# Kernel tuning notes

Hardware: AMD Instinct MI355X
Metric: run time of the kernel (lower is better)

Reference implementation:

```python
import jax, jax.numpy as jnp
import numpy as np

B, Q, E = 4, 1024, 1024
N_HEAD, D_HEAD = 16, 64
LN_EPS = 1e-3  # keras LayerNormalization default


def rel_shift(x):
    # x: [b, q, k, n] -> Transformer-XL relative shift along k axis
    b, q, k, n = x.shape
    x = jnp.pad(x, ((0, 0), (0, 0), (1, 0), (0, 0)))
    x = x.reshape(b, k + 1, q, n)[:, 1:]
    return x.reshape(b, q, k, n)


def setup_inputs() -> dict:
    key = jax.random.key(0)
    ks = jax.random.split(key, 12)
    s = 0.02
    w = jax.random.normal(ks[0], (B, Q, E), jnp.float32)
    r = jax.random.normal(ks[1], (Q, E), jnp.float32)
    r_w_bias = jax.random.normal(ks[2], (N_HEAD, D_HEAD), jnp.float32) * s
    r_r_bias = jax.random.normal(ks[3], (N_HEAD, D_HEAD), jnp.float32) * s
    # causal mask: 1 where j > i (masked), float as in original
    idx = jnp.arange(Q)
    attn_mask = (idx[None, :] > idx[:, None]).astype(jnp.float32)
    Wq = jax.random.normal(ks[4], (E, N_HEAD * D_HEAD), jnp.float32) * s
    Wk = jax.random.normal(ks[5], (E, N_HEAD * D_HEAD), jnp.float32) * s
    Wv = jax.random.normal(ks[6], (E, N_HEAD * D_HEAD), jnp.float32) * s
    Wr = jax.random.normal(ks[7], (E, N_HEAD * D_HEAD), jnp.float32) * s
    Wo = jax.random.normal(ks[8], (N_HEAD * D_HEAD, E), jnp.float32) * s
    gamma = jnp.ones((E,), jnp.float32)
    beta = jnp.zeros((E,), jnp.float32)
    return {"w": w, "r": r, "r_w_bias": r_w_bias, "r_r_bias": r_r_bias,
            "attn_mask": attn_mask, "Wq": Wq, "Wk": Wk, "Wv": Wv, "Wr": Wr,
            "Wo": Wo, "gamma": gamma, "beta": beta}


def reference(w, r, r_w_bias, r_r_bias, attn_mask, Wq, Wk, Wv, Wr, Wo, gamma, beta):
    b, q_len, embed = w.shape
    r_len = r.shape[0]
    # QKV / R projections (use_bias=False)
    q = (w @ Wq).reshape(b, q_len, N_HEAD, D_HEAD)
    k = (w @ Wk).reshape(b, q_len, N_HEAD, D_HEAD)
    v = (w @ Wv).reshape(b, q_len, N_HEAD, D_HEAD)
    rp = (r @ Wr).reshape(r_len, N_HEAD, D_HEAD)
    rw_q = q + r_w_bias  # [b,i,n,d]
    rr_q = q + r_r_bias
    AC = jnp.einsum('bind,bjnd->bijn', rw_q, k)
    BD = jnp.einsum('bind,jnd->bijn', rr_q, rp)
    BD = rel_shift(BD)
    attention = (AC + BD) / jnp.sqrt(jnp.float32(embed))
    m = attn_mask[None, :, :, None]
    attention = attention * (1.0 - m) - 1e30 * m
    attn_score = jax.nn.softmax(attention, axis=-2)  # softmax over j (key axis)
    out = jnp.einsum('bijn,bjnd->bind', attn_score, v)
    out = out.reshape(b, q_len, N_HEAD * D_HEAD) @ Wo
    x = w + out
    # keras LayerNormalization over last axis
    mu = jnp.mean(x, axis=-1, keepdims=True)
    var = jnp.var(x, axis=-1, keepdims=True)
    x = (x - mu) * jax.lax.rsqrt(var + LN_EPS) * gamma + beta
    return x
```

## Files before the change

### kernel.cpp

```cpp
#include <hip/hip_runtime.h>
#include <math.h>

#define BQ 4
#define SEQ 1024
#define EMB 1024
#define NH 16
#define DH 64
#define LN_EPS 1e-3f

typedef unsigned short u16;
typedef __attribute__((ext_vector_type(8))) unsigned short ushort8;
typedef __attribute__((ext_vector_type(4))) unsigned short ushort4v;
typedef __attribute__((ext_vector_type(8))) __bf16 bf16x8;
typedef __attribute__((ext_vector_type(4))) float f32x4;

__device__ __forceinline__ u16 f2bf(float f) {
  union { float f; unsigned u; } v;
  v.f = f;
  unsigned u = v.u;
  u += 0x7FFF + ((u >> 16) & 1);
  return (u16)(u >> 16);
}
__device__ __forceinline__ float bf2f(u16 h) {
  union { unsigned u; float f; } v;
  v.u = ((unsigned)h) << 16;
  return v.f;
}
__device__ __forceinline__ bf16x8 as_bf(ushort8 v) {
  union { ushort8 u; bf16x8 b; } x;
  x.u = v;
  return x.b;
}
__device__ __forceinline__ f32x4 mfma16(ushort8 a, ushort8 b, f32x4 c) {
  return __builtin_amdgcn_mfma_f32_16x16x32_bf16(as_bf(a), as_bf(b), c, 0, 0, 0);
}
__device__ __forceinline__ void gload16(const u16* g, u16* l) {
  __builtin_amdgcn_global_load_lds(
      (const __attribute__((address_space(1))) void*)g,
      (__attribute__((address_space(3))) void*)l, 16, 0, 0);
}

__global__ __launch_bounds__(256) void prep_kernel(
    const float* __restrict__ w, const float* __restrict__ r,
    const float* __restrict__ Wq, const float* __restrict__ Wk,
    const float* __restrict__ Wv, const float* __restrict__ Wr,
    const float* __restrict__ Wo, u16* __restrict__ wbf,
    u16* __restrict__ rbf, u16* __restrict__ WqkvT, u16* __restrict__ WrT,
    u16* __restrict__ WoT) {
  __shared__ u16 tile[32][33];
  const int bid = blockIdx.x;
  const int tid = threadIdx.x;
  if (bid < 5120) {
    const float* src = (bid < 4096) ? w : r;
    u16* dst = (bid < 4096) ? wbf : rbf;
    const int base = (bid < 4096) ? bid : bid - 4096;
    const int idx = (base * 256 + tid) * 4;
    const float4 v = *(const float4*)&src[idx];
    ushort4v o;
    o[0] = f2bf(v.x);
    o[1] = f2bf(v.y);
    o[2] = f2bf(v.z);
    o[3] = f2bf(v.w);
    *(ushort4v*)&dst[idx] = o;
  } else {
    const int t = bid - 5120;
    const int z = t >> 10;
    const int tt = t & 1023;
    const float* src = (z == 0) ? Wq : (z == 1) ? Wk : (z == 2) ? Wv
                       : (z == 3) ? Wr : Wo;
    u16* dst = (z < 3) ? (WqkvT + (size_t)z * 1024 * 1024)
               : (z == 3) ? WrT : WoT;
    const int k0 = (tt >> 5) * 32, n0 = (tt & 31) * 32;
    const int rr = tid >> 3, c4 = tid & 7;
    const float4 v =
        *(const float4*)&src[(size_t)(k0 + rr) * 1024 + n0 + c4 * 4];
    tile[rr][c4 * 4 + 0] = f2bf(v.x);
    tile[rr][c4 * 4 + 1] = f2bf(v.y);
    tile[rr][c4 * 4 + 2] = f2bf(v.z);
    tile[rr][c4 * 4 + 3] = f2bf(v.w);
    __syncthreads();
    ushort4v o;
#pragma unroll
    for (int e = 0; e < 4; ++e) o[e] = tile[c4 * 4 + e][rr];
    *(ushort4v*)&dst[(size_t)(n0 + rr) * 1024 + k0 + c4 * 4] = o;
  }
}

__device__ __forceinline__ void gemm_core(const u16* __restrict__ A,
                                          const u16* __restrict__ Bt, int bm0,
                                          int bn0, u16* As, u16* Bs, int tid,
                                          f32x4 acc[4][4]) {
  const int quad = (tid >> 4) & 3, colL = tid & 15;
  const int wv = tid >> 6;
  const int wr = wv >> 1, wc = wv & 1;
  const int xs = colL & 7;
  for (int k0 = 0; k0 < 1024; k0 += 64) {
#pragma unroll
    for (int rr = 0; rr < 4; ++rr) {
      const int c = rr * 256 + tid;
      const int row = c >> 3, kc = c & 7;
      const int g = kc ^ (row & 7);
      gload16(&A[(size_t)(bm0 + row) * 1024 + k0 + g * 8], &As[c * 8]);
      gload16(&Bt[(size_t)(bn0 + row) * 1024 + k0 + g * 8], &Bs[c * 8]);
    }
    __syncthreads();
#pragma unroll
    for (int kh = 0; kh < 2; ++kh) {
      const int xo = ((kh * 4 + quad) ^ xs) * 8;
      ushort8 af[4], bf[4];
#pragma unroll
      for (int t = 0; t < 4; ++t) {
        af[t] = *(const ushort8*)&As[(wr * 64 + t * 16 + colL) * 64 + xo];
        bf[t] = *(const ushort8*)&Bs[(wc * 64 + t * 16 + colL) * 64 + xo];
      }
#pragma unroll
      for (int i = 0; i < 4; ++i)
#pragma unroll
        for (int j = 0; j < 4; ++j)
          acc[i][j] = mfma16(af[i], bf[j], acc[i][j]);
    }
    __syncthreads();
  }
}

__global__ __launch_bounds__(256) void gemm_qkvrp(
    const u16* __restrict__ wbf, const u16* __restrict__ WqkvT,
    const u16* __restrict__ rbf, const u16* __restrict__ WrT,
    u16* __restrict__ qk, u16* __restrict__ vT, u16* __restrict__ rpb) {
  __shared__ u16 As[128 * 64];
  __shared__ u16 Bs[128 * 64];
  const int bid = blockIdx.x;
  const int tid = threadIdx.x;
  const bool isR = (bid >= 768);
  const u16* A = isR ? rbf : wbf;
  const u16* Bt = isR ? WrT : WqkvT;
  const int bm0 = isR ? ((bid - 768) >> 3) * 128 : (bid / 24) * 128;
  const int bn0 = isR ? ((bid - 768) & 7) * 128 : (bid % 24) * 128;

  f32x4 acc[4][4] = {};
  gemm_core(A, Bt, bm0, bn0, As, Bs, tid, acc);

  const int quad = (tid >> 4) & 3, colL = tid & 15;
  const int wv = tid >> 6;
  const int wr = wv >> 1, wc = wv & 1;
  const bool vpart = !isR && (bn0 >= 2048);
#pragma unroll
  for (int i = 0; i < 4; ++i) {
    const int grow0 = bm0 + wr * 64 + i * 16 + quad * 4;
#pragma unroll
    for (int j = 0; j < 4; ++j) {
      const int gcol = bn0 + wc * 64 + j * 16 + colL;
      if (vpart) {
        const size_t base =
            ((size_t)(grow0 >> 10) * 1024 + (gcol - 2048)) * 1024 +
            (grow0 & 1023);
        ushort4v o;
#pragma unroll
        for (int e = 0; e < 4; ++e) o[e] = f2bf(acc[i][j][e]);
        *(ushort4v*)&vT[base] = o;
      } else {
        u16* dst = isR ? rpb : qk;
        const int Nld = isR ? 1024 : 2048;
#pragma unroll
        for (int e = 0; e < 4; ++e)
          dst[(size_t)(grow0 + e) * Nld + gcol] = f2bf(acc[i][j][e]);
      }
    }
  }
}

__global__ __launch_bounds__(256) void gemm_wo(const u16* __restrict__ A,
                                               const u16* __restrict__ Bt,
                                               const float* __restrict__ res,
                                               float* __restrict__ C) {
  __shared__ u16 As[128 * 64];
  __shared__ u16 Bs[128 * 64];
  const int tid = threadIdx.x;
  const int bm0 = blockIdx.y * 128, bn0 = blockIdx.x * 128;
  f32x4 acc[4][4] = {};
  gemm_core(A, Bt, bm0, bn0, As, Bs, tid, acc);
  const int quad = (tid >> 4) & 3, colL = tid & 15;
  const int wv = tid >> 6;
  const int wr = wv >> 1, wc = wv & 1;
#pragma unroll
  for (int i = 0; i < 4; ++i) {
    const int grow0 = bm0 + wr * 64 + i * 16 + quad * 4;
#pragma unroll
    for (int j = 0; j < 4; ++j) {
      const int gcol = bn0 + wc * 64 + j * 16 + colL;
#pragma unroll
      for (int e = 0; e < 4; ++e) {
        const size_t off = (size_t)(grow0 + e) * 1024 + gcol;
        C[off] = acc[i][j][e] + res[off];
      }
    }
  }
}

__global__ __launch_bounds__(256, 3) void attn_mfma(
    const u16* __restrict__ qk,
    const u16* __restrict__ vT,
    const u16* __restrict__ rp,
    const float* __restrict__ rwb, const float* __restrict__ rrb,
    u16* __restrict__ obuf) {
  __shared__ u16 smem[22016];
  u16* ks = smem;
  u16* vs = smem + 4096;
  u16* rs = smem + 8192;
  u16* Ps = smem + 16384;

  const int L = blockIdx.x;
  const int b = L & 3;
  const int hn = (L >> 2) & 15;
  const int ph = L >> 6;
  const int itile = (ph < 8) ? ph : 23 - ph;
  const int i0 = itile * 64;
  const int tid = threadIdx.x;
  const int wv = tid >> 6;
  const int lane = tid & 63;
  const int quad = (tid >> 4) & 3, colL = tid & 15;
  u16* Psw = Ps + wv * 16 * 88;
  const int xo0 = (quad ^ (colL & 7)) * 8;
  const int xo1 = ((4 + quad) ^ (colL & 7)) * 8;

  ushort8 qw[2], qr[2];
  {
    const size_t qrow = (size_t)(b * SEQ + i0 + wv * 16 + colL) * 2048;
#pragma unroll
    for (int kh = 0; kh < 2; ++kh) {
      const int dof = hn * 64 + kh * 32 + quad * 8;
      const ushort8 qv = *(const ushort8*)&qk[qrow + dof];
      const float4 w0 = *(const float4*)&rwb[dof];
      const float4 w1 = *(const float4*)&rwb[dof + 4];
      const float4 r0 = *(const float4*)&rrb[dof];
      const float4 r1 = *(const float4*)&rrb[dof + 4];
      const float wb[8] = {w0.x, w0.y, w0.z, w0.w, w1.x, w1.y, w1.z, w1.w};
      const float rb[8] = {r0.x, r0.y, r0.z, r0.w, r1.x, r1.y, r1.z, r1.w};
#pragma unroll
      for (int e = 0; e < 8; ++e) {
        const float qf = bf2f(qv[e]);
        qw[kh][e] = f2bf(qf + wb[e]);
        qr[kh][e] = f2bf(qf + rb[e]);
      }
    }
  }

  {
    const int pb0 = SEQ - 64 - i0;
#pragma unroll
    for (int rr = 0; rr < 2; ++rr) {
      const int c = rr * 256 + tid;
      const int row = c >> 3, gp = c & 7;
      const int g = gp ^ (row & 7);
      gload16(&rp[(size_t)(pb0 + row) * 1024 + hn * 64 + g * 8], &rs[c * 8]);
    }
  }

  f32x4 oacc[4] = {};
  float l_part[4] = {0.f, 0.f, 0.f, 0.f};

  for (int j0 = 0; j0 <= i0; j0 += 64) {
    const int parity = (j0 >> 6) & 1;
    __syncthreads();
#pragma unroll
    for (int rr = 0; rr < 2; ++rr) {
      const int c = rr * 256 + tid;
      const int row = c >> 3, gp = c & 7;
      const int g = gp ^ (row & 7);
      gload16(&qk[(size_t)(b * SEQ + j0 + row) * 2048 + 1024 + hn * 64 + g * 8],
              &ks[c * 8]);
    }
#pragma unroll
    for (int rr = 0; rr < 2; ++rr) {
      const int c = rr * 256 + tid;
      const int d = c >> 3, gp = c & 7;
      const int g = gp ^ (d & 7);
      gload16(&vT[(size_t)(b * SEQ + hn * 64 + d) * 1024 + j0 + g * 8],
              &vs[c * 8]);
    }
    {
      const int pb64 = SEQ - i0 + j0;
      u16* rsH = rs + (parity ^ 1) * 4096;
#pragma unroll
      for (int rr = 0; rr < 2; ++rr) {
        const int c = rr * 256 + tid;
        const int row = c >> 3, gp = c & 7;
        const int g = gp ^ (row & 7);
        int p = pb64 + row;
        p = (p < SEQ) ? p : SEQ - 1;
        gload16(&rp[(size_t)p * 1024 + hn * 64 + g * 8], &rsH[c * 8]);
      }
    }
    __syncthreads();

    f32x4 sAC[4] = {};
#pragma unroll
    for (int jt = 0; jt < 4; ++jt) {
      const int rbase = (jt * 16 + colL) * 64;
      sAC[jt] = mfma16(qw[0], *(const ushort8*)&ks[rbase + xo0], sAC[jt]);
      sAC[jt] = mfma16(qw[1], *(const ushort8*)&ks[rbase + xo1], sAC[jt]);
    }
    f32x4 bd[5];
#pragma unroll
    for (int u = 0; u < 5; ++u) {
      const int tt = 3 - wv + u;
      const int half = ((tt >> 2) ^ parity) & 1;
      const int rbase = half * 4096 + ((tt & 3) * 16 + colL) * 64;
      f32x4 t = {};
      t = mfma16(qr[0], *(const ushort8*)&rs[rbase + xo0], t);
      t = mfma16(qr[1], *(const ushort8*)&rs[rbase + xo1], t);
      bd[u] = t;
    }

#pragma unroll
    for (int r = 0; r < 4; ++r) {
      const int lr = quad * 4 + r;
      const int ig = i0 + wv * 16 + lr;
      const int src = (lane & 48) | ((colL + 15 - lr) & 15);
      float Rv[5];
#pragma unroll
      for (int u = 0; u < 5; ++u) Rv[u] = __shfl(bd[u][r], src, 64);
#pragma unroll
      for (int jt = 0; jt < 4; ++jt) {
        const float bdv = (colL > lr) ? Rv[jt + 1] : Rv[jt];
        const float s = (sAC[jt][r] + bdv) * 0.03125f;
        const float pv = (j0 + jt * 16 + colL <= ig) ? __expf(s - 6.0f) : 0.0f;
        l_part[r] += pv;
        Psw[lr * 88 + jt * 16 + colL] = f2bf(pv);
      }
    }

    const int prow = colL * 88;
#pragma unroll
    for (int dt = 0; dt < 4; ++dt) {
      const int vbase = (dt * 16 + colL) * 64;
      oacc[dt] = mfma16(*(const ushort8*)&Psw[prow + quad * 8],
                        *(const ushort8*)&vs[vbase + xo0], oacc[dt]);
      oacc[dt] = mfma16(*(const ushort8*)&Psw[prow + 32 + quad * 8],
                        *(const ushort8*)&vs[vbase + xo1], oacc[dt]);
    }
  }

#pragma unroll
  for (int r = 0; r < 4; ++r) {
    float l = l_part[r];
    l += __shfl_xor(l, 1);
    l += __shfl_xor(l, 2);
    l += __shfl_xor(l, 4);
    l += __shfl_xor(l, 8);
    const float invl = 1.0f / l;
    const size_t grow =
        (size_t)(b * SEQ + i0 + wv * 16 + quad * 4 + r) * 1024 + hn * 64;
#pragma unroll
    for (int dt = 0; dt < 4; ++dt)
      obuf[grow + dt * 16 + colL] = f2bf(oacc[dt][r] * invl);
  }
}

__global__ __launch_bounds__(256) void ln_kernel(const float* __restrict__ x,
                                                 const float* __restrict__ gamma,
                                                 const float* __restrict__ beta,
                                                 float* __restrict__ out) {
  const int row = blockIdx.x;
  const int tid = threadIdx.x;
  const float4 xv = *(const float4*)&x[(size_t)row * EMB + tid * 4];
  float sum = xv.x + xv.y + xv.z + xv.w;
  float ss = xv.x * xv.x + xv.y * xv.y + xv.z * xv.z + xv.w * xv.w;
#pragma unroll
  for (int off = 1; off < 64; off <<= 1) {
    sum += __shfl_xor(sum, off);
    ss += __shfl_xor(ss, off);
  }
  __shared__ float s1[4], s2[4];
  if ((tid & 63) == 0) {
    s1[tid >> 6] = sum;
    s2[tid >> 6] = ss;
  }
  __syncthreads();
  sum = s1[0] + s1[1] + s1[2] + s1[3];
  ss = s2[0] + s2[1] + s2[2] + s2[3];
  const float mu = sum * (1.f / EMB);
  const float var = ss * (1.f / EMB) - mu * mu;
  const float rstd = rsqrtf(var + LN_EPS);
  const float4 g = *(const float4*)&gamma[tid * 4];
  const float4 be = *(const float4*)&beta[tid * 4];
  float4 o;
  o.x = (xv.x - mu) * rstd * g.x + be.x;
  o.y = (xv.y - mu) * rstd * g.y + be.y;
  o.z = (xv.z - mu) * rstd * g.z + be.z;
  o.w = (xv.w - mu) * rstd * g.w + be.w;
  *(float4*)&out[(size_t)row * EMB + tid * 4] = o;
}

extern "C" void kernel_launch(void* const* d_in, const int* in_sizes, int n_in,
                              void* d_out, int out_size, void* d_ws,
                              size_t ws_size, hipStream_t stream) {
  const float* w = (const float*)d_in[0];
  const float* r = (const float*)d_in[1];
  const float* rwb = (const float*)d_in[2];
  const float* rrb = (const float*)d_in[3];
  const float* Wq = (const float*)d_in[5];
  const float* Wk = (const float*)d_in[6];
  const float* Wv = (const float*)d_in[7];
  const float* Wr = (const float*)d_in[8];
  const float* Wo = (const float*)d_in[9];
  const float* gamma = (const float*)d_in[10];
  const float* beta = (const float*)d_in[11];
  float* outp = (float*)d_out;

  char* wsb = (char*)d_ws;
  u16* wbf = (u16*)(wsb);
  u16* rbf = (u16*)(wsb + ((size_t)8 << 20));
  u16* WqkvT = (u16*)(wsb + ((size_t)10 << 20));
  u16* WrT = (u16*)(wsb + ((size_t)16 << 20));
  u16* WoT = (u16*)(wsb + ((size_t)18 << 20));
  u16* qk = (u16*)(wsb + ((size_t)20 << 20));
  u16* vT = (u16*)(wsb + ((size_t)36 << 20));
  u16* rpb = (u16*)(wsb + ((size_t)44 << 20));
  u16* obuf = (u16*)(wsb + ((size_t)10 << 20));

  const dim3 blk(256);
  prep_kernel<<<10240, blk, 0, stream>>>(w, r, Wq, Wk, Wv, Wr, Wo, wbf, rbf,
                                         WqkvT, WrT, WoT);
  gemm_qkvrp<<<832, blk, 0, stream>>>(wbf, WqkvT, rbf, WrT, qk, vT, rpb);
  attn_mfma<<<1024, blk, 0, stream>>>(qk, vT, rpb, rwb, rrb, obuf);
  gemm_wo<<<dim3(8, 32), blk, 0, stream>>>(obuf, WoT, w, outp);
  ln_kernel<<<BQ * SEQ, blk, 0, stream>>>(outp, gamma, beta, outp);
}
```

Measured before the change: 225.2 us.

## Double-buffer GEMM shared-memory tiles to overlap global loads with MFMA

```diff
diff --git a/kernel.cpp b/kernel.cpp
--- a/kernel.cpp
+++ b/kernel.cpp
@@ -86,40 +86,57 @@
   }
 }
 
-__device__ __forceinline__ void gemm_core(const u16* __restrict__ A,
-                                          const u16* __restrict__ Bt, int bm0,
-                                          int bn0, u16* As, u16* Bs, int tid,
-                                          f32x4 acc[4][4]) {
+__device__ __forceinline__ void gemm_stage(const u16* __restrict__ A,
+                                           const u16* __restrict__ Bt, int bm0,
+                                           int bn0, int k0, u16* As, u16* Bs,
+                                           int tid) {
+#pragma unroll
+  for (int rr = 0; rr < 4; ++rr) {
+    const int c = rr * 256 + tid;
+    const int row = c >> 3, kc = c & 7;
+    const int g = kc ^ (row & 7);
+    gload16(&A[(size_t)(bm0 + row) * 1024 + k0 + g * 8], &As[c * 8]);
+    gload16(&Bt[(size_t)(bn0 + row) * 1024 + k0 + g * 8], &Bs[c * 8]);
+  }
+}
+
+__device__ __forceinline__ void gemm_compute(const u16* As, const u16* Bs,
+                                             int tid, f32x4 acc[4][4]) {
   const int quad = (tid >> 4) & 3, colL = tid & 15;
   const int wv = tid >> 6;
   const int wr = wv >> 1, wc = wv & 1;
   const int xs = colL & 7;
-  for (int k0 = 0; k0 < 1024; k0 += 64) {
-#pragma unroll
-    for (int rr = 0; rr < 4; ++rr) {
-      const int c = rr * 256 + tid;
-      const int row = c >> 3, kc = c & 7;
-      const int g = kc ^ (row & 7);
-      gload16(&A[(size_t)(bm0 + row) * 1024 + k0 + g * 8], &As[c * 8]);
-      gload16(&Bt[(size_t)(bn0 + row) * 1024 + k0 + g * 8], &Bs[c * 8]);
-    }
+#pragma unroll
+  for (int kh = 0; kh < 2; ++kh) {
+    const int xo = ((kh * 4 + quad) ^ xs) * 8;
+    ushort8 af[4], bf[4];
+#pragma unroll
+    for (int t = 0; t < 4; ++t) {
+      af[t] = *(const ushort8*)&As[(wr * 64 + t * 16 + colL) * 64 + xo];
+      bf[t] = *(const ushort8*)&Bs[(wc * 64 + t * 16 + colL) * 64 + xo];
+    }
+#pragma unroll
+    for (int i = 0; i < 4; ++i)
+#pragma unroll
+      for (int j = 0; j < 4; ++j) acc[i][j] = mfma16(af[i], bf[j], acc[i][j]);
+  }
+}
+
+__device__ __forceinline__ void gemm_core(const u16* __restrict__ A,
+                                          const u16* __restrict__ Bt, int bm0,
+                                          int bn0, u16* smem, int tid,
+                                          f32x4 acc[4][4]) {
+  u16* As[2] = {smem, smem + 16384};
+  u16* Bs[2] = {smem + 8192, smem + 24576};
+  gemm_stage(A, Bt, bm0, bn0, 0, As[0], Bs[0], tid);
+#pragma unroll 2
+  for (int it = 0; it < 16; ++it) {
+    const int cur = it & 1;
     __syncthreads();
-#pragma unroll
-    for (int kh = 0; kh < 2; ++kh) {
-      const int xo = ((kh * 4 + quad) ^ xs) * 8;
-      ushort8 af[4], bf[4];
-#pragma unroll
-      for (int t = 0; t < 4; ++t) {
-        af[t] = *(const ushort8*)&As[(wr * 64 + t * 16 + colL) * 64 + xo];
-        bf[t] = *(const ushort8*)&Bs[(wc * 64 + t * 16 + colL) * 64 + xo];
-      }
-#pragma unroll
-      for (int i = 0; i < 4; ++i)
-#pragma unroll
-        for (int j = 0; j < 4; ++j)
-          acc[i][j] = mfma16(af[i], bf[j], acc[i][j]);
-    }
-    __syncthreads();
+    if (it < 15)
+      gemm_stage(A, Bt, bm0, bn0, (it + 1) * 64, As[cur ^ 1], Bs[cur ^ 1],
+                 tid);
+    gemm_compute(As[cur], Bs[cur], tid, acc);
   }
 }
 
@@ -127,8 +144,7 @@
     const u16* __restrict__ wbf, const u16* __restrict__ WqkvT,
     const u16* __restrict__ rbf, const u16* __restrict__ WrT,
     u16* __restrict__ qk, u16* __restrict__ vT, u16* __restrict__ rpb) {
-  __shared__ u16 As[128 * 64];
-  __shared__ u16 Bs[128 * 64];
+  __shared__ u16 smem[32768];
   const int bid = blockIdx.x;
   const int tid = threadIdx.x;
   const bool isR = (bid >= 768);
@@ -138,7 +154,7 @@
   const int bn0 = isR ? ((bid - 768) & 7) * 128 : (bid % 24) * 128;
 
   f32x4 acc[4][4] = {};
-  gemm_core(A, Bt, bm0, bn0, As, Bs, tid, acc);
+  gemm_core(A, Bt, bm0, bn0, smem, tid, acc);
 
   const int quad = (tid >> 4) & 3, colL = tid & 15;
   const int wv = tid >> 6;
@@ -173,12 +189,11 @@
                                                const u16* __restrict__ Bt,
                                                const float* __restrict__ res,
                                                float* __restrict__ C) {
-  __shared__ u16 As[128 * 64];
-  __shared__ u16 Bs[128 * 64];
+  __shared__ u16 smem[32768];
   const int tid = threadIdx.x;
   const int bm0 = blockIdx.y * 128, bn0 = blockIdx.x * 128;
   f32x4 acc[4][4] = {};
-  gemm_core(A, Bt, bm0, bn0, As, Bs, tid, acc);
+  gemm_core(A, Bt, bm0, bn0, smem, tid, acc);
   const int quad = (tid >> 4) & 3, colL = tid & 15;
   const int wv = tid >> 6;
   const int wr = wv >> 1, wc = wv & 1;
```

After: 201.8 us. 1.12x faster.
